# Performance work log

Measured on AMD Instinct MI355X. Metric: run time of the kernel, lower is better.

## Reference

```python
import jax, jax.numpy as jnp
import numpy as np

B, MC, U, N, DIN, DOUT, E = 2048, 4, 20000, 100000, 128, 128, 65536
RES_RATE = 0.9


def setup_inputs() -> dict:
    key = jax.random.key(0)
    ks = jax.random.split(key, 12)
    s = 1.0 / np.sqrt(DIN)
    return {
        'nodes': jax.random.randint(ks[0], (B,), 0, N),
        'unique_ids': jax.random.randint(ks[1], (U,), 0, N),
        'row_idx': jnp.repeat(jnp.arange(B), E // B),
        'layer_idx': jax.random.randint(ks[2], (E,), 0, MC),
        'col_idx': jax.random.randint(ks[3], (E,), 0, U),
        'agg_table': jax.random.normal(ks[4], (N, DIN), jnp.float32),
        'ff_table': jax.random.normal(ks[5], (N, DIN), jnp.float32),
        'Wv_agg': jax.random.normal(ks[6], (DIN, DOUT), jnp.float32) * s,
        'Wv_ff': jax.random.normal(ks[7], (DIN, DOUT), jnp.float32) * s,
        'Wk': jax.random.normal(ks[8], (DIN, DOUT), jnp.float32) * s,
        'Wq': jax.random.normal(ks[9], (DIN, DOUT), jnp.float32) * s,
        'mu_w': jax.random.normal(ks[10], (2 * DOUT, 1), jnp.float32) * s,
    }


def reference(nodes, unique_ids, row_idx, layer_idx, col_idx,
              agg_table, ff_table, Wv_agg, Wv_ff, Wk, Wq, mu_w):
    # feature lookups (the 'features' encoder returns (agg_attr, ff_attr))
    embed_agg = agg_table[unique_ids]            # [U, DIN]
    self_agg_raw = agg_table[nodes]              # [B, DIN]
    self_ff_raw = ff_table[nodes]                # [B, DIN]

    # highway K/Q from raw self features
    self_pair = jnp.stack((self_agg_raw, self_ff_raw), axis=1)  # [B, 2, DIN]
    K = self_pair @ Wk                            # [B, 2, DOUT]
    Q = self_pair @ Wq                            # [B, 2, DOUT]

    embed_agg_v = embed_agg @ Wv_agg              # [U, DOUT]
    self_agg = self_agg_raw @ Wv_agg              # [B, DOUT]

    # dense normalized neighbor mask [B, MC, U]
    mask = jnp.zeros((B, MC, U), jnp.float32).at[row_idx, layer_idx, col_idx].set(1.0)
    cnt = mask.sum(-1, keepdims=True)
    mask = mask / jnp.where(cnt == 0, 1.0, cnt)
    neigh = jnp.einsum('bmu,ud->bmd', mask, embed_agg_v)  # [B, MC, DOUT]

    # persona combination
    coef = jnp.concatenate(
        (jnp.broadcast_to(self_agg[:, None, :], (B, MC, DOUT)), neigh), axis=-1)
    norm = jnp.maximum(jnp.linalg.norm(coef, axis=-1, keepdims=True), 1e-12)
    coef = jax.nn.softmax((coef / norm) @ mu_w, axis=1)    # [B, MC, 1]
    neigh_sum = jnp.sum(neigh * coef, axis=1)              # [B, DOUT]
    self_agg = (self_agg + neigh_sum) / 2.0

    # feed-forward branch + highway attention
    self_ff = self_ff_raw @ Wv_ff                          # [B, DOUT]
    V = jnp.stack((self_agg, self_ff), axis=1)             # [B, 2, DOUT]
    scores = jax.nn.softmax(jnp.einsum('bid,bjd->bij', K, Q) / DOUT, axis=-1)
    new = jnp.einsum('bij,bjd->bid', scores, V)            # [B, 2, DOUT]
    self_agg = RES_RATE * self_agg + (1 - RES_RATE) * new[:, 0]
    self_ff = RES_RATE * self_ff + (1 - RES_RATE) * new[:, 1]
    return jax.nn.elu(self_agg), jax.nn.elu(self_ff)
```

## Files before the change

kernel.cpp:

```cpp
#include <hip/hip_runtime.h>

typedef unsigned short u16;
typedef unsigned int u32;

#define NB 2048
#define NMC 4
#define NU 20000
#define ND 128
#define EPB 32

#define GEMM_BR 128
#define EMBED_BLOCKS 157

__global__ __launch_bounds__(256) void gemm_all(
    const float* __restrict__ agg, const float* __restrict__ ff,
    const float* __restrict__ Wv_agg, const float* __restrict__ Wv_ff,
    const float* __restrict__ Wk, const float* __restrict__ Wq,
    const int* __restrict__ uids, const int* __restrict__ nodes,
    float* __restrict__ embed_v,
    float* __restrict__ selfA, float* __restrict__ selfF,
    float* __restrict__ K0, float* __restrict__ K1,
    float* __restrict__ Q0, float* __restrict__ Q1)
{
    __shared__ float Ws[64 * ND];
    __shared__ float As[64 * ND];

    const int bx = blockIdx.x;
    const int t  = threadIdx.x;

    const float* table = agg; const int* ids = uids; const float* W = Wv_agg;
    float* outp = embed_v;
    int M, r0;
    if (bx < EMBED_BLOCKS) {
        M = NU; r0 = bx * GEMM_BR;
    } else {
        int z = bx - EMBED_BLOCKS;
        int mode = z >> 4;
        r0 = (z & 15) * GEMM_BR;
        M = NB; ids = nodes;
        switch (mode) {
            case 0: table = agg; W = Wv_agg; outp = selfA; break;
            case 1: table = agg; W = Wk;     outp = K0;    break;
            case 2: table = agg; W = Wq;     outp = Q0;    break;
            case 3: table = ff;  W = Wv_ff;  outp = selfF; break;
            case 4: table = ff;  W = Wk;     outp = K1;    break;
            default: table = ff; W = Wq;     outp = Q1;    break;
        }
    }

    const int rs = t >> 1;
    const int hs = t & 1;
    int srow = r0 + rs;
    const int id = ids[srow < M ? srow : (M - 1)];

    const int rt = (t >> 4) * 8;
    const int ct = (t & 15) * 8;

    float acc[8][8];
    #pragma unroll
    for (int i = 0; i < 8; i++)
        #pragma unroll
        for (int j = 0; j < 8; j++) acc[i][j] = 0.f;

    for (int kk = 0; kk < ND; kk += 64) {
        {
            const float4* src = (const float4*)(W + kk * ND);
            float4* dst = (float4*)Ws;
            #pragma unroll
            for (int i = 0; i < 8; i++) dst[t + i * 256] = src[t + i * 256];
        }
        {
            const float4* src = (const float4*)(table + (size_t)id * ND + kk + hs * 32);
            #pragma unroll
            for (int i = 0; i < 8; i++) {
                float4 v = src[i];
                int k = hs * 32 + i * 4;
                As[(k + 0) * GEMM_BR + rs] = v.x;
                As[(k + 1) * GEMM_BR + rs] = v.y;
                As[(k + 2) * GEMM_BR + rs] = v.z;
                As[(k + 3) * GEMM_BR + rs] = v.w;
            }
        }
        __syncthreads();

        #pragma unroll 2
        for (int k = 0; k < 64; k++) {
            float4 a0 = *(const float4*)&As[k * GEMM_BR + rt];
            float4 a1 = *(const float4*)&As[k * GEMM_BR + rt + 4];
            float4 w0 = *(const float4*)&Ws[k * ND + ct];
            float4 w1 = *(const float4*)&Ws[k * ND + ct + 4];
            float a[8] = {a0.x, a0.y, a0.z, a0.w, a1.x, a1.y, a1.z, a1.w};
            float w[8] = {w0.x, w0.y, w0.z, w0.w, w1.x, w1.y, w1.z, w1.w};
            #pragma unroll
            for (int i = 0; i < 8; i++)
                #pragma unroll
                for (int j = 0; j < 8; j++) acc[i][j] += a[i] * w[j];
        }
        __syncthreads();
    }

    #pragma unroll
    for (int i = 0; i < 8; i++) {
        int row = r0 + rt + i;
        if (row >= M) continue;
        float4* o = (float4*)&outp[(size_t)row * ND + ct];
        o[0] = make_float4(acc[i][0], acc[i][1], acc[i][2], acc[i][3]);
        o[1] = make_float4(acc[i][4], acc[i][5], acc[i][6], acc[i][7]);
    }
}

__global__ __launch_bounds__(128) void finalize(
    const int* __restrict__ layer_idx, const int* __restrict__ col_idx,
    const float* __restrict__ embed_v,
    const float* __restrict__ selfA, const float* __restrict__ selfF,
    const float* __restrict__ K0, const float* __restrict__ K1,
    const float* __restrict__ Q0, const float* __restrict__ Q1,
    const float* __restrict__ mu_w, float* __restrict__ out)
{
    const int b = blockIdx.x;
    const int t = threadIdx.x;

    __shared__ int   Ls[EPB], Cs[EPB], cnt[NMC];
    __shared__ float keepf[EPB];
    __shared__ float red[14 * 2];
    __shared__ float bc[8];

    if (t < NMC) cnt[t] = 0;
    if (t < EPB) {
        Ls[t] = layer_idx[b * EPB + t];
        Cs[t] = col_idx[b * EPB + t];
    }
    __syncthreads();
    if (t < EPB) {
        int l = Ls[t], c = Cs[t];
        int kp = 1;
        for (int j = 0; j < t; j++)
            if (Ls[j] == l && Cs[j] == c) { kp = 0; break; }
        keepf[t] = kp ? 1.0f : 0.0f;
        if (kp) atomicAdd(&cnt[l], 1);
    }
    __syncthreads();

    float a0 = 0.f, a1 = 0.f, a2 = 0.f, a3 = 0.f;
    #pragma unroll
    for (int e = 0; e < EPB; e++) {
        float v = embed_v[(size_t)Cs[e] * ND + t];
        float vk = v * keepf[e];
        int l = Ls[e];
        a0 += (l == 0) ? vk : 0.f;
        a1 += (l == 1) ? vk : 0.f;
        a2 += (l == 2) ? vk : 0.f;
        a3 += (l == 3) ? vk : 0.f;
    }
    float inv0 = cnt[0] > 0 ? 1.f / (float)cnt[0] : 0.f;
    float inv1 = cnt[1] > 0 ? 1.f / (float)cnt[1] : 0.f;
    float inv2 = cnt[2] > 0 ? 1.f / (float)cnt[2] : 0.f;
    float inv3 = cnt[3] > 0 ? 1.f / (float)cnt[3] : 0.f;
    float n0 = a0 * inv0, n1 = a1 * inv1, n2 = a2 * inv2, n3 = a3 * inv3;

    const size_t base = (size_t)b * ND + t;
    float sA = selfA[base];
    float sF = selfF[base];
    float k0 = K0[base], k1 = K1[base], q0 = Q0[base], q1 = Q1[base];
    float mu0 = mu_w[t], mu1 = mu_w[ND + t];

    float vals[14] = {
        sA * sA, sA * mu0,
        n0 * n0, n1 * n1, n2 * n2, n3 * n3,
        n0 * mu1, n1 * mu1, n2 * mu1, n3 * mu1,
        k0 * q0, k0 * q1, k1 * q0, k1 * q1
    };
    const int lane = t & 63, wv = t >> 6;
    #pragma unroll
    for (int s = 0; s < 14; s++) {
        float v = vals[s];
        #pragma unroll
        for (int off = 32; off; off >>= 1) v += __shfl_xor(v, off);
        if (lane == 0) red[s * 2 + wv] = v;
    }
    __syncthreads();

    if (t == 0) {
        float sn = red[0] + red[1];
        float ds = red[2] + red[3];
        float sc[NMC], mx = -1e30f;
        #pragma unroll
        for (int m = 0; m < NMC; m++) {
            float nn = red[(2 + m) * 2] + red[(2 + m) * 2 + 1];
            float dn = red[(6 + m) * 2] + red[(6 + m) * 2 + 1];
            float nrm = fmaxf(sqrtf(sn + nn), 1e-12f);
            sc[m] = (ds + dn) / nrm;
            mx = fmaxf(mx, sc[m]);
        }
        float se = 0.f, ee[NMC];
        #pragma unroll
        for (int m = 0; m < NMC; m++) { ee[m] = expf(sc[m] - mx); se += ee[m]; }
        #pragma unroll
        for (int m = 0; m < NMC; m++) bc[m] = ee[m] / se;

        float s00 = (red[20] + red[21]) * (1.f / 128.f);
        float s01 = (red[22] + red[23]) * (1.f / 128.f);
        float s10 = (red[24] + red[25]) * (1.f / 128.f);
        float s11 = (red[26] + red[27]) * (1.f / 128.f);
        float m0 = fmaxf(s00, s01), e00 = expf(s00 - m0), e01 = expf(s01 - m0);
        float d0 = e00 + e01;
        bc[4] = e00 / d0; bc[5] = e01 / d0;
        float m1 = fmaxf(s10, s11), e10 = expf(s10 - m1), e11 = expf(s11 - m1);
        float d1 = e10 + e11;
        bc[6] = e10 / d1; bc[7] = e11 / d1;
    }
    __syncthreads();

    float nsum = n0 * bc[0] + n1 * bc[1] + n2 * bc[2] + n3 * bc[3];
    float sa1 = (sA + nsum) * 0.5f;
    float new0 = bc[4] * sa1 + bc[5] * sF;
    float new1 = bc[6] * sa1 + bc[7] * sF;
    float o0 = 0.9f * sa1 + 0.1f * new0;
    float o1 = 0.9f * sF  + 0.1f * new1;
    o0 = o0 > 0.f ? o0 : (expf(o0) - 1.f);
    o1 = o1 > 0.f ? o1 : (expf(o1) - 1.f);
    out[base] = o0;
    out[(size_t)NB * ND + base] = o1;
}

extern "C" void kernel_launch(void* const* d_in, const int* in_sizes, int n_in,
                              void* d_out, int out_size, void* d_ws, size_t ws_size,
                              hipStream_t stream) {
    const int* nodes  = (const int*)d_in[0];
    const int* uids   = (const int*)d_in[1];
    const int* layer  = (const int*)d_in[3];
    const int* col    = (const int*)d_in[4];
    const float* agg    = (const float*)d_in[5];
    const float* ff     = (const float*)d_in[6];
    const float* Wv_agg = (const float*)d_in[7];
    const float* Wv_ff  = (const float*)d_in[8];
    const float* Wk     = (const float*)d_in[9];
    const float* Wq     = (const float*)d_in[10];
    const float* mu     = (const float*)d_in[11];

    float* embed_v = (float*)d_ws;
    float* selfA   = embed_v + (size_t)NU * ND;
    float* selfF   = selfA + (size_t)NB * ND;
    float* K0      = selfF + (size_t)NB * ND;
    float* K1      = K0 + (size_t)NB * ND;
    float* Q0      = K1 + (size_t)NB * ND;
    float* Q1      = Q0 + (size_t)NB * ND;

    float* out = (float*)d_out;

    gemm_all<<<EMBED_BLOCKS + 6 * (NB / GEMM_BR), 256, 0, stream>>>(
        agg, ff, Wv_agg, Wv_ff, Wk, Wq, uids, nodes,
        embed_v, selfA, selfF, K0, K1, Q0, Q1);

    finalize<<<NB, 128, 0, stream>>>(
        layer, col, embed_v, selfA, selfF, K0, K1, Q0, Q1, mu, out);
}
```

Baseline: 163.4 us.

## Switch gather-GEMM to bf16 MFMA with pre-transposed bf16 weights

Adds a small prep kernel that transposes the four weight matrices and converts them to bf16. The gather GEMM now converts gathered rows to bf16 in LDS and computes with 16x16x32 bf16 MFMA instructions instead of scalar FP32 FMAs. The goal is to cut the compute time of the projection GEMMs, at the cost of an extra kernel launch and reduced precision, which may hurt accuracy against the fp32 reference.

```diff
diff --git a/kernel.cpp b/kernel.cpp
--- a/kernel.cpp
+++ b/kernel.cpp
@@ -1,4 +1,5 @@
 #include <hip/hip_runtime.h>
+#include <hip/hip_bf16.h>
 
 typedef unsigned short u16;
 typedef unsigned int u32;
@@ -9,103 +10,150 @@
 #define ND 128
 #define EPB 32
 
-#define GEMM_BR 128
+typedef __attribute__((ext_vector_type(8))) short bf16x8;
+typedef __attribute__((ext_vector_type(4))) float f32x4;
+
+__device__ __forceinline__ u32 pack_bf16(float a, float b) {
+    __hip_bfloat162 h = __float22bfloat162_rn(make_float2(a, b));
+    return *(u32*)&h;
+}
+
+__global__ __launch_bounds__(256) void prep_wt(
+    const float* __restrict__ Wv_agg, const float* __restrict__ Wk,
+    const float* __restrict__ Wq, const float* __restrict__ Wv_ff,
+    u16* __restrict__ WT)
+{
+    __shared__ float Wl[16 * ND];
+    const int m = blockIdx.x >> 3;
+    const int ks = (blockIdx.x & 7) * 16;
+    const int t = threadIdx.x;
+
+    const float* W = (m == 0) ? Wv_agg : (m == 1) ? Wk : (m == 2) ? Wq : Wv_ff;
+    const float4* src = (const float4*)(W + ks * ND);
+    float4* dst = (float4*)Wl;
+    dst[t * 2] = src[t * 2];
+    dst[t * 2 + 1] = src[t * 2 + 1];
+    __syncthreads();
+
+    const int c = t >> 1, kh = t & 1;
+    float v[8];
+    #pragma unroll
+    for (int j = 0; j < 8; j++) v[j] = Wl[(kh * 8 + j) * ND + c];
+    uint4 pk;
+    pk.x = pack_bf16(v[0], v[1]);
+    pk.y = pack_bf16(v[2], v[3]);
+    pk.z = pack_bf16(v[4], v[5]);
+    pk.w = pack_bf16(v[6], v[7]);
+    *(uint4*)&WT[((size_t)(m * ND + c)) * ND + ks + kh * 8] = pk;
+}
+
+#define LDSK 72
 #define EMBED_BLOCKS 157
 
 __global__ __launch_bounds__(256) void gemm_all(
     const float* __restrict__ agg, const float* __restrict__ ff,
-    const float* __restrict__ Wv_agg, const float* __restrict__ Wv_ff,
-    const float* __restrict__ Wk, const float* __restrict__ Wq,
+    const u16* __restrict__ WT,
     const int* __restrict__ uids, const int* __restrict__ nodes,
     float* __restrict__ embed_v,
     float* __restrict__ selfA, float* __restrict__ selfF,
     float* __restrict__ K0, float* __restrict__ K1,
     float* __restrict__ Q0, float* __restrict__ Q1)
 {
-    __shared__ float Ws[64 * ND];
-    __shared__ float As[64 * ND];
+    __shared__ u16 As[ND * LDSK];
+    __shared__ u16 Bs[ND * LDSK];
 
     const int bx = blockIdx.x;
     const int t  = threadIdx.x;
 
-    const float* table = agg; const int* ids = uids; const float* W = Wv_agg;
+    const float* table = agg; const int* ids = uids; int wtm = 0;
     float* outp = embed_v;
     int M, r0;
     if (bx < EMBED_BLOCKS) {
-        M = NU; r0 = bx * GEMM_BR;
+        M = NU; r0 = bx * 128;
     } else {
         int z = bx - EMBED_BLOCKS;
         int mode = z >> 4;
-        r0 = (z & 15) * GEMM_BR;
+        r0 = (z & 15) * 128;
         M = NB; ids = nodes;
         switch (mode) {
-            case 0: table = agg; W = Wv_agg; outp = selfA; break;
-            case 1: table = agg; W = Wk;     outp = K0;    break;
-            case 2: table = agg; W = Wq;     outp = Q0;    break;
-            case 3: table = ff;  W = Wv_ff;  outp = selfF; break;
-            case 4: table = ff;  W = Wk;     outp = K1;    break;
-            default: table = ff; W = Wq;     outp = Q1;    break;
-        }
-    }
-
-    const int rs = t >> 1;
-    const int hs = t & 1;
+            case 0: table = agg; wtm = 0; outp = selfA; break;
+            case 1: table = agg; wtm = 1; outp = K0;    break;
+            case 2: table = agg; wtm = 2; outp = Q0;    break;
+            case 3: table = ff;  wtm = 3; outp = selfF; break;
+            case 4: table = ff;  wtm = 1; outp = K1;    break;
+            default: table = ff; wtm = 2; outp = Q1;    break;
+        }
+    }
+
+    const int rs = t >> 1, hs = t & 1;
     int srow = r0 + rs;
     const int id = ids[srow < M ? srow : (M - 1)];
-
-    const int rt = (t >> 4) * 8;
-    const int ct = (t & 15) * 8;
-
-    float acc[8][8];
-    #pragma unroll
-    for (int i = 0; i < 8; i++)
-        #pragma unroll
-        for (int j = 0; j < 8; j++) acc[i][j] = 0.f;
-
-    for (int kk = 0; kk < ND; kk += 64) {
+    const float* arow = table + (size_t)id * ND;
+    const u16* wrow = WT + ((size_t)(wtm * ND + rs)) * ND;
+
+    const int w = t >> 6, lane = t & 63, q = lane >> 4, li = lane & 15;
+
+    f32x4 acc[2][8];
+    #pragma unroll
+    for (int i = 0; i < 2; i++)
+        #pragma unroll
+        for (int j = 0; j < 8; j++) acc[i][j] = (f32x4){0.f, 0.f, 0.f, 0.f};
+
+    for (int pass = 0; pass < 2; pass++) {
+        const int k0 = pass * 64;
         {
-            const float4* src = (const float4*)(W + kk * ND);
-            float4* dst = (float4*)Ws;
-            #pragma unroll
-            for (int i = 0; i < 8; i++) dst[t + i * 256] = src[t + i * 256];
+            const float4* asrc = (const float4*)(arow + k0 + hs * 32);
+            #pragma unroll
+            for (int i = 0; i < 4; i++) {
+                float4 v0 = asrc[2 * i], v1 = asrc[2 * i + 1];
+                uint4 pk;
+                pk.x = pack_bf16(v0.x, v0.y);
+                pk.y = pack_bf16(v0.z, v0.w);
+                pk.z = pack_bf16(v1.x, v1.y);
+                pk.w = pack_bf16(v1.z, v1.w);
+                *(uint4*)&As[rs * LDSK + hs * 32 + i * 8] = pk;
+            }
         }
         {
-            const float4* src = (const float4*)(table + (size_t)id * ND + kk + hs * 32);
-            #pragma unroll
-            for (int i = 0; i < 8; i++) {
-                float4 v = src[i];
-                int k = hs * 32 + i * 4;
-                As[(k + 0) * GEMM_BR + rs] = v.x;
-                As[(k + 1) * GEMM_BR + rs] = v.y;
-                As[(k + 2) * GEMM_BR + rs] = v.z;
-                As[(k + 3) * GEMM_BR + rs] = v.w;
+            const uint4* bsrc = (const uint4*)(wrow + k0 + hs * 32);
+            #pragma unroll
+            for (int i = 0; i < 4; i++)
+                *(uint4*)&Bs[rs * LDSK + hs * 32 + i * 8] = bsrc[i];
+        }
+        __syncthreads();
+
+        #pragma unroll
+        for (int c = 0; c < 2; c++) {
+            const int kk = c * 32 + q * 8;
+            bf16x8 af[2], bfr[8];
+            #pragma unroll
+            for (int tr = 0; tr < 2; tr++)
+                af[tr] = *(const bf16x8*)&As[(w * 32 + tr * 16 + li) * LDSK + kk];
+            #pragma unroll
+            for (int tc = 0; tc < 8; tc++)
+                bfr[tc] = *(const bf16x8*)&Bs[(tc * 16 + li) * LDSK + kk];
+            #pragma unroll
+            for (int tr = 0; tr < 2; tr++)
+                #pragma unroll
+                for (int tc = 0; tc < 8; tc++)
+                    acc[tr][tc] = __builtin_amdgcn_mfma_f32_16x16x32_bf16(
+                        af[tr], bfr[tc], acc[tr][tc], 0, 0, 0);
+        }
+        __syncthreads();
+    }
+
+    #pragma unroll
+    for (int tr = 0; tr < 2; tr++) {
+        const int rloc = w * 32 + tr * 16 + q * 4;
+        #pragma unroll
+        for (int r = 0; r < 4; r++) {
+            const int row = r0 + rloc + r;
+            if (row < M) {
+                #pragma unroll
+                for (int tc = 0; tc < 8; tc++)
+                    outp[(size_t)row * ND + tc * 16 + li] = acc[tr][tc][r];
             }
         }
-        __syncthreads();
-
-        #pragma unroll 2
-        for (int k = 0; k < 64; k++) {
-            float4 a0 = *(const float4*)&As[k * GEMM_BR + rt];
-            float4 a1 = *(const float4*)&As[k * GEMM_BR + rt + 4];
-            float4 w0 = *(const float4*)&Ws[k * ND + ct];
-            float4 w1 = *(const float4*)&Ws[k * ND + ct + 4];
-            float a[8] = {a0.x, a0.y, a0.z, a0.w, a1.x, a1.y, a1.z, a1.w};
-            float w[8] = {w0.x, w0.y, w0.z, w0.w, w1.x, w1.y, w1.z, w1.w};
-            #pragma unroll
-            for (int i = 0; i < 8; i++)
-                #pragma unroll
-                for (int j = 0; j < 8; j++) acc[i][j] += a[i] * w[j];
-        }
-        __syncthreads();
-    }
-
-    #pragma unroll
-    for (int i = 0; i < 8; i++) {
-        int row = r0 + rt + i;
-        if (row >= M) continue;
-        float4* o = (float4*)&outp[(size_t)row * ND + ct];
-        o[0] = make_float4(acc[i][0], acc[i][1], acc[i][2], acc[i][3]);
-        o[1] = make_float4(acc[i][4], acc[i][5], acc[i][6], acc[i][7]);
     }
 }
 
@@ -238,7 +286,8 @@
     const float* Wq     = (const float*)d_in[10];
     const float* mu     = (const float*)d_in[11];
 
-    float* embed_v = (float*)d_ws;
+    u16*   WT      = (u16*)d_ws;
+    float* embed_v = (float*)((char*)d_ws + 4 * ND * ND * sizeof(u16));
     float* selfA   = embed_v + (size_t)NU * ND;
     float* selfF   = selfA + (size_t)NB * ND;
     float* K0      = selfF + (size_t)NB * ND;
@@ -248,8 +297,10 @@
 
     float* out = (float*)d_out;
 
-    gemm_all<<<EMBED_BLOCKS + 6 * (NB / GEMM_BR), 256, 0, stream>>>(
-        agg, ff, Wv_agg, Wv_ff, Wk, Wq, uids, nodes,
+    prep_wt<<<32, 256, 0, stream>>>(Wv_agg, Wk, Wq, Wv_ff, WT);
+
+    gemm_all<<<EMBED_BLOCKS + 6 * (NB / 128), 256, 0, stream>>>(
+        agg, ff, WT, uids, nodes,
         embed_v, selfA, selfF, K0, K1, Q0, Q1);
 
     finalize<<<NB, 128, 0, stream>>>(
```

Result: faster. 152.6 us (-6.6%).
